# Kernel optimization log

Hardware: AMD Instinct MI355X
Metric: run time of the kernel (lower is better)

## Reference

```python
import jax, jax.numpy as jnp
import numpy as np
from jax import lax

# DCNv2 (ModulatedDeformConvPack) constants per init_kwargs
STRIDE, PAD, DIL, DG, KH, KW = 1, 1, 1, 1, 3, 3
K = KH * KW


def setup_inputs() -> dict:
    key = jax.random.key(0)
    k0, k1, k2 = jax.random.split(key, 3)
    B, C, H, W = 2, 64, 128, 128
    O = 64
    x = jax.random.normal(k0, (B, C, H, W), jnp.float32)
    weight = jax.random.normal(k1, (O, C, KH, KW), jnp.float32) / np.sqrt(C * KH * KW)
    bias = jnp.zeros((O,), jnp.float32)
    # small scale so predicted offsets stay within a few pixels (realistic trained DCN)
    offset_w = jax.random.normal(k2, (DG * 3 * K, C, KH, KW), jnp.float32) * 0.01
    offset_b = jnp.zeros((DG * 3 * K,), jnp.float32)
    return {"x": x, "weight": weight, "bias": bias, "offset_w": offset_w, "offset_b": offset_b}


def _modulated_deform_conv(x, weight, bias, offset_w, offset_b):
    B, C, H, W = x.shape
    O = weight.shape[0]
    # 1) offset/mask prediction conv (standard conv, same geometry as main conv)
    off = lax.conv_general_dilated(
        x, offset_w, window_strides=(STRIDE, STRIDE), padding=((PAD, PAD), (PAD, PAD)),
        rhs_dilation=(DIL, DIL), dimension_numbers=("NCHW", "OIHW", "NCHW"))
    off = off + offset_b[None, :, None, None]
    Ho, Wo = off.shape[2], off.shape[3]
    o1, o2, m = jnp.split(off, 3, axis=1)
    dy = o1.reshape(B, DG, K, Ho, Wo)
    dx = o2.reshape(B, DG, K, Ho, Wo)
    mask = jax.nn.sigmoid(m).reshape(B, DG, K, Ho, Wo)

    # 2) sampling positions: p = p0 + k*dil - pad + offset
    ki, kj = jnp.meshgrid(jnp.arange(KH), jnp.arange(KW), indexing="ij")
    base_y = (jnp.arange(Ho) * STRIDE - PAD)[None, :, None] + (ki.reshape(K) * DIL)[:, None, None]  # (K,Ho,1)
    base_x = (jnp.arange(Wo) * STRIDE - PAD)[None, None, :] + (kj.reshape(K) * DIL)[:, None, None]  # (K,1,Wo)
    py = base_y[None, None].astype(x.dtype) + dy  # (B,DG,K,Ho,Wo)
    px = base_x[None, None].astype(x.dtype) + dx

    y0 = jnp.floor(py)
    x0 = jnp.floor(px)
    wy = py - y0  # fractional weights
    wx = px - x0
    y0i = y0.astype(jnp.int32)
    x0i = x0.astype(jnp.int32)

    Cg = C // DG
    xg = x.reshape(B, DG, Cg, H * W)

    def corner(yi, xi):
        valid = ((yi >= 0) & (yi < H) & (xi >= 0) & (xi < W)).astype(x.dtype)  # zero-pad outside
        idx = jnp.clip(yi, 0, H - 1) * W + jnp.clip(xi, 0, W - 1)  # (B,DG,K,Ho,Wo)
        gather = lambda xf, id_: xf[:, id_]  # (Cg, K, Ho, Wo)
        vals = jax.vmap(jax.vmap(gather))(xg, idx)  # (B,DG,Cg,K,Ho,Wo)
        return vals * valid[:, :, None]

    wy_ = wy[:, :, None]
    wx_ = wx[:, :, None]
    samp = (corner(y0i, x0i) * (1 - wy_) * (1 - wx_)
            + corner(y0i, x0i + 1) * (1 - wy_) * wx_
            + corner(y0i + 1, x0i) * wy_ * (1 - wx_)
            + corner(y0i + 1, x0i + 1) * wy_ * wx_)
    samp = samp * mask[:, :, None]  # modulation
    samp = samp.reshape(B, C, K, Ho, Wo)

    # 3) contraction with conv weight (groups=1)
    out = jnp.einsum("bckhw,ock->bohw", samp, weight.reshape(O, C, K))
    return out + bias[None, :, None, None]


def reference(x, weight, bias, offset_w, offset_b):
    return _modulated_deform_conv(x, weight, bias, offset_w, offset_b)
```

## Files before the change

kernel.cpp:

```cpp
#include <hip/hip_runtime.h>
#include <hip/hip_bf16.h>

typedef __attribute__((ext_vector_type(8))) short bf16x8;
typedef __attribute__((ext_vector_type(4))) float f32x4;

#define Bc 2
#define Cc 64
#define Hc 128
#define Wc 128
#define Oc 64
#define NOFF 27
#define HWc (Hc * Wc)

__device__ __forceinline__ short f2bf(float f) {
    __hip_bfloat16 h = __float2bfloat16(f);
    return __builtin_bit_cast(short, h);
}
__device__ __forceinline__ float bf2f(short s) {
    __hip_bfloat16 h = __builtin_bit_cast(__hip_bfloat16, s);
    return __bfloat162float(h);
}

__global__ __launch_bounds__(256) void prep_kernel(
    const float* __restrict__ x, const float* __restrict__ w, const float* __restrict__ ow,
    short* __restrict__ xT, short* __restrict__ Ahi, short* __restrict__ Ohi) {
    int bid = blockIdx.x;
    int t = threadIdx.x;
    if (bid < 512) {
        int b = bid >> 8, rem = bid & 255;
        int h = rem >> 1, w0 = (rem & 1) << 6;
        __shared__ float tile[64][68];
        {
            int c = t >> 2, sub = t & 3;
            const float* src = x + ((size_t)(b * Cc + c) * Hc + h) * Wc + w0 + sub * 16;
#pragma unroll
            for (int j = 0; j < 4; ++j)
                *(float4*)&tile[c][sub * 16 + 4 * j] = *(const float4*)(src + 4 * j);
        }
        __syncthreads();
        {
            int ww = t >> 2, cs = (t & 3) << 4;
            short* dst = xT + (((size_t)(b * Hc + h)) * Wc + w0 + ww) * Cc + cs;
            bf16x8 v0, v1;
#pragma unroll
            for (int j = 0; j < 8; ++j) {
                v0[j] = f2bf(tile[cs + j][ww]);
                v1[j] = f2bf(tile[cs + 8 + j][ww]);
            }
            *(bf16x8*)(dst) = v0;
            *(bf16x8*)(dst + 8) = v1;
        }
    } else {
        int idx = (bid - 512) * 256 + t;
        const int NM = 4 * 18 * 64 * 8;
        const int NO = 2 * 18 * 64 * 8;
        if (idx < NM) {
            int j = idx & 7, lane = (idx >> 3) & 63, ks = (idx >> 9) % 18, mt = idx / 9216;
            int o  = mt * 16 + (lane & 15);
            int kk = ks >> 1;
            int c  = (ks & 1) * 32 + (lane >> 4) * 8 + j;
            Ahi[idx] = f2bf(w[(o * Cc + c) * 9 + kk]);
        } else if (idx < NM + NO) {
            int t2 = idx - NM;
            int j = t2 & 7, lane = (t2 >> 3) & 63, ks = (t2 >> 9) % 18, mt = t2 / 9216;
            int o  = mt * 16 + (lane & 15);
            int kk = ks >> 1;
            int c  = (ks & 1) * 32 + (lane >> 4) * 8 + j;
            Ohi[t2] = f2bf((o < NOFF) ? ow[(o * Cc + c) * 9 + kk] : 0.f);
        }
    }
}

__global__ __launch_bounds__(256, 2) void fused_dcn_kernel(
    const short* __restrict__ xT,
    const short* __restrict__ Ahi, const short* __restrict__ Ohi,
    const float* __restrict__ bias, const float* __restrict__ obias,
    float* __restrict__ out) {
    int bid = blockIdx.x;
    int b = bid >> 8, rem = bid & 255;
    int h = rem >> 1, w0 = (rem & 1) << 6;
    int tid = threadIdx.x;
    int lane = tid & 63, wv = tid >> 6;
    int n_loc = lane & 15, quad = lane >> 4;
    int p_glob = wv * 16 + n_loc;
    int wpix = w0 + p_glob;
    int cb0 = quad * 8, cb1 = 32 + quad * 8;

    __shared__ __align__(16) short Asm[2 * 18 * 64 * 8];
    __shared__ float4 wgt[576];
    __shared__ int4   sidx[576];
    __shared__ float  tmp[NOFF * 64];

    const short* xb = xT + (size_t)b * HWc * Cc;

    f32x4 oacc0 = {0.f, 0.f, 0.f, 0.f}, oacc1 = {0.f, 0.f, 0.f, 0.f};
    bf16x8 s1A[2], s1B[2];
    {
        int yc = min(max(h - 1, 0), Hc - 1);
        int xc = min(max(wpix - 1, 0), Wc - 1);
        const short* base = xb + ((size_t)yc * Wc + xc) * Cc;
        s1A[0] = *(const bf16x8*)(base + cb0);
        s1A[1] = *(const bf16x8*)(base + cb1);
    }
#pragma unroll
    for (int kk = 0; kk < 9; ++kk) {
        bf16x8* cur = (kk & 1) ? s1B : s1A;
        bf16x8* nxt = (kk & 1) ? s1A : s1B;
        if (kk < 8) {
            int kk2 = kk + 1;
            int yc = min(max(h + kk2 / 3 - 1, 0), Hc - 1);
            int xc = min(max(wpix + kk2 % 3 - 1, 0), Wc - 1);
            const short* base = xb + ((size_t)yc * Wc + xc) * Cc;
            nxt[0] = *(const bf16x8*)(base + cb0);
            nxt[1] = *(const bf16x8*)(base + cb1);
        }
        int y = h + kk / 3 - 1, xw = wpix + kk % 3 - 1;
        bool val = ((unsigned)y < (unsigned)Hc) && ((unsigned)xw < (unsigned)Wc);
        bf16x8 z = {0, 0, 0, 0, 0, 0, 0, 0};
        bf16x8 b0 = val ? cur[0] : z;
        bf16x8 b1 = val ? cur[1] : z;
#pragma unroll
        for (int ks = 0; ks < 2; ++ks) {
            bf16x8 bf = ks ? b1 : b0;
            int ksg = kk * 2 + ks;
            bf16x8 ah0 = *(const bf16x8*)(Ohi + ((0 * 18 + ksg) * 64 + lane) * 8);
            oacc0 = __builtin_amdgcn_mfma_f32_16x16x32_bf16(ah0, bf, oacc0, 0, 0, 0);
            bf16x8 ah1 = *(const bf16x8*)(Ohi + ((1 * 18 + ksg) * 64 + lane) * 8);
            oacc1 = __builtin_amdgcn_mfma_f32_16x16x32_bf16(ah1, bf, oacc1, 0, 0, 0);
        }
    }
    {
        int mrow = quad * 4;
#pragma unroll
        for (int r = 0; r < 4; ++r) {
            int oc = mrow + r;
            if (oc < NOFF) tmp[oc * 64 + p_glob] = oacc0[r] + obias[oc];
            int oc2 = 16 + mrow + r;
            if (oc2 < NOFF) tmp[oc2 * 64 + p_glob] = oacc1[r] + obias[oc2];
        }
    }
    for (int i = tid; i < 2304; i += 256)
        *((bf16x8*)Asm + i) = *((const bf16x8*)Ahi + i);
    __syncthreads();

    for (int t = tid; t < 576; t += 256) {
        int k = t >> 6, p = t & 63;
        float dy = tmp[k * 64 + p];
        float dx = tmp[(9 + k) * 64 + p];
        float mm = tmp[(18 + k) * 64 + p];
        float m  = 1.f / (1.f + __expf(-mm));
        float py = (float)(h - 1 + k / 3) + dy;
        float px = (float)(w0 + p - 1 + k % 3) + dx;
        float y0f = floorf(py), x0f = floorf(px);
        float fy = py - y0f, fx = px - x0f;
        int y0 = (int)y0f, x0i = (int)x0f;
        float vy0 = (y0 >= 0 && y0 < Hc) ? 1.f : 0.f;
        float vy1 = (y0 + 1 >= 0 && y0 + 1 < Hc) ? 1.f : 0.f;
        float vx0 = (x0i >= 0 && x0i < Wc) ? 1.f : 0.f;
        float vx1 = (x0i + 1 >= 0 && x0i + 1 < Wc) ? 1.f : 0.f;
        wgt[t] = make_float4((1.f - fy) * (1.f - fx) * m * vy0 * vx0,
                             (1.f - fy) * fx         * m * vy0 * vx1,
                             fy         * (1.f - fx) * m * vy1 * vx0,
                             fy         * fx         * m * vy1 * vx1);
        int cy0 = min(max(y0, 0), Hc - 1) * Wc;
        int cy1 = min(max(y0 + 1, 0), Hc - 1) * Wc;
        int cx0 = min(max(x0i, 0), Wc - 1);
        int cx1 = min(max(x0i + 1, 0), Wc - 1);
        sidx[t] = make_int4(cy0 + cx0, cy0 + cx1, cy1 + cx0, cy1 + cx1);
    }
    __syncthreads();

    f32x4 acc[4] = {{0.f, 0.f, 0.f, 0.f}, {0.f, 0.f, 0.f, 0.f},
                    {0.f, 0.f, 0.f, 0.f}, {0.f, 0.f, 0.f, 0.f}};
    bf16x8 bufA[8], bufB[8];
    float4 w4 = wgt[p_glob];
    {
        int4 id = sidx[p_glob];
        const short* c00 = xb + (size_t)id.x * Cc;
        const short* c01 = xb + (size_t)id.y * Cc;
        const short* c10 = xb + (size_t)id.z * Cc;
        const short* c11 = xb + (size_t)id.w * Cc;
        bufA[0] = *(const bf16x8*)(c00 + cb0); bufA[1] = *(const bf16x8*)(c00 + cb1);
        bufA[2] = *(const bf16x8*)(c01 + cb0); bufA[3] = *(const bf16x8*)(c01 + cb1);
        bufA[4] = *(const bf16x8*)(c10 + cb0); bufA[5] = *(const bf16x8*)(c10 + cb1);
        bufA[6] = *(const bf16x8*)(c11 + cb0); bufA[7] = *(const bf16x8*)(c11 + cb1);
    }
#pragma unroll
    for (int kk = 0; kk < 9; ++kk) {
        bf16x8* cur = (kk & 1) ? bufB : bufA;
        bf16x8* nxt = (kk & 1) ? bufA : bufB;
        float4 w4n = w4;
        if (kk < 8) {
            int4 idn = sidx[(kk + 1) * 64 + p_glob];
            w4n = wgt[(kk + 1) * 64 + p_glob];
            const short* c00 = xb + (size_t)idn.x * Cc;
            const short* c01 = xb + (size_t)idn.y * Cc;
            const short* c10 = xb + (size_t)idn.z * Cc;
            const short* c11 = xb + (size_t)idn.w * Cc;
            nxt[0] = *(const bf16x8*)(c00 + cb0); nxt[1] = *(const bf16x8*)(c00 + cb1);
            nxt[2] = *(const bf16x8*)(c01 + cb0); nxt[3] = *(const bf16x8*)(c01 + cb1);
            nxt[4] = *(const bf16x8*)(c10 + cb0); nxt[5] = *(const bf16x8*)(c10 + cb1);
            nxt[6] = *(const bf16x8*)(c11 + cb0); nxt[7] = *(const bf16x8*)(c11 + cb1);
        }
        bf16x8 b0, b1;
#pragma unroll
        for (int j = 0; j < 8; ++j) {
            float s0 = w4.x * bf2f(cur[0][j]) + w4.y * bf2f(cur[2][j])
                     + w4.z * bf2f(cur[4][j]) + w4.w * bf2f(cur[6][j]);
            float s1 = w4.x * bf2f(cur[1][j]) + w4.y * bf2f(cur[3][j])
                     + w4.z * bf2f(cur[5][j]) + w4.w * bf2f(cur[7][j]);
            b0[j] = f2bf(s0);
            b1[j] = f2bf(s1);
        }
#pragma unroll
        for (int ks = 0; ks < 2; ++ks) {
            bf16x8 bf = ks ? b1 : b0;
            int ksg = kk * 2 + ks;
            bf16x8 a0 = *(const bf16x8*)(Asm + ((0 * 18 + ksg) * 64 + lane) * 8);
            acc[0] = __builtin_amdgcn_mfma_f32_16x16x32_bf16(a0, bf, acc[0], 0, 0, 0);
            bf16x8 a1 = *(const bf16x8*)(Asm + ((1 * 18 + ksg) * 64 + lane) * 8);
            acc[1] = __builtin_amdgcn_mfma_f32_16x16x32_bf16(a1, bf, acc[1], 0, 0, 0);
            bf16x8 a2 = *(const bf16x8*)(Ahi + ((2 * 18 + ksg) * 64 + lane) * 8);
            acc[2] = __builtin_amdgcn_mfma_f32_16x16x32_bf16(a2, bf, acc[2], 0, 0, 0);
            bf16x8 a3 = *(const bf16x8*)(Ahi + ((3 * 18 + ksg) * 64 + lane) * 8);
            acc[3] = __builtin_amdgcn_mfma_f32_16x16x32_bf16(a3, bf, acc[3], 0, 0, 0);
        }
        w4 = w4n;
    }

    int mrow = quad * 4;
    float* ob = out + ((size_t)b * Oc * Hc + h) * Wc + w0 + p_glob;
#pragma unroll
    for (int mt = 0; mt < 4; ++mt)
#pragma unroll
        for (int r = 0; r < 4; ++r) {
            int o = mt * 16 + mrow + r;
            ob[(size_t)o * HWc] = acc[mt][r] + bias[o];
        }
}

extern "C" void kernel_launch(void* const* d_in, const int* in_sizes, int n_in,
                              void* d_out, int out_size, void* d_ws, size_t ws_size,
                              hipStream_t stream) {
    const float* x        = (const float*)d_in[0];
    const float* weight   = (const float*)d_in[1];
    const float* bias     = (const float*)d_in[2];
    const float* offset_w = (const float*)d_in[3];
    const float* offset_b = (const float*)d_in[4];
    float* out = (float*)d_out;

    char* ws = (char*)d_ws;
    short* xT  = (short*)(ws + 0);
    short* Ahi = (short*)(ws + 4194304);
    short* Ohi = (short*)(ws + 4268032);

    prep_kernel<<<512 + 216, 256, 0, stream>>>(x, weight, offset_w, xT, Ahi, Ohi);
    fused_dcn_kernel<<<Bc * Hc * 2, 256, 0, stream>>>(xT, Ahi, Ohi, bias, offset_b, out);
}
```

Measured before the change: 99.36 us.

## Split kernel taps across two wave groups with LDS reduction (split-K)

Doubles the block to 512 threads, with each half handling a subset of the 9 kernel taps (0-3 and 4-8) in both the offset conv and the deformable sampling and MFMA stage. Partial accumulators are reduced through shared memory before the offset post-processing and again before the output store. This is meant to raise wave-level parallelism and hide gather latency on a grid of only 512 blocks. In exchange it adds extra barriers, LDS traffic for the reductions, and uneven work between the two halves.

```diff
diff --git a/kernel.cpp b/kernel.cpp
--- a/kernel.cpp
+++ b/kernel.cpp
@@ -71,7 +71,111 @@
     }
 }
 
-__global__ __launch_bounds__(256, 2) void fused_dcn_kernel(
+template<int KB, int KE>
+__device__ __forceinline__ void stage1_taps(
+    const short* __restrict__ xb, const short* __restrict__ Ohi,
+    int h, int wpix, int lane, int cb0, int cb1, f32x4& oacc0, f32x4& oacc1) {
+    bf16x8 bA[2], bB[2];
+    {
+        int yc = min(max(h + KB / 3 - 1, 0), Hc - 1);
+        int xc = min(max(wpix + KB % 3 - 1, 0), Wc - 1);
+        const short* base = xb + ((size_t)yc * Wc + xc) * Cc;
+        bA[0] = *(const bf16x8*)(base + cb0);
+        bA[1] = *(const bf16x8*)(base + cb1);
+    }
+#pragma unroll
+    for (int kk = KB; kk < KE; ++kk) {
+        bf16x8* cur = ((kk - KB) & 1) ? bB : bA;
+        bf16x8* nxt = ((kk - KB) & 1) ? bA : bB;
+        if (kk < KE - 1) {
+            int kk2 = kk + 1;
+            int yc = min(max(h + kk2 / 3 - 1, 0), Hc - 1);
+            int xc = min(max(wpix + kk2 % 3 - 1, 0), Wc - 1);
+            const short* base = xb + ((size_t)yc * Wc + xc) * Cc;
+            nxt[0] = *(const bf16x8*)(base + cb0);
+            nxt[1] = *(const bf16x8*)(base + cb1);
+        }
+        int y = h + kk / 3 - 1, xw = wpix + kk % 3 - 1;
+        bool val = ((unsigned)y < (unsigned)Hc) && ((unsigned)xw < (unsigned)Wc);
+        bf16x8 z = {0, 0, 0, 0, 0, 0, 0, 0};
+        bf16x8 b0 = val ? cur[0] : z;
+        bf16x8 b1 = val ? cur[1] : z;
+#pragma unroll
+        for (int ks = 0; ks < 2; ++ks) {
+            bf16x8 bf = ks ? b1 : b0;
+            int ksg = kk * 2 + ks;
+            bf16x8 ah0 = *(const bf16x8*)(Ohi + ((0 * 18 + ksg) * 64 + lane) * 8);
+            oacc0 = __builtin_amdgcn_mfma_f32_16x16x32_bf16(ah0, bf, oacc0, 0, 0, 0);
+            bf16x8 ah1 = *(const bf16x8*)(Ohi + ((1 * 18 + ksg) * 64 + lane) * 8);
+            oacc1 = __builtin_amdgcn_mfma_f32_16x16x32_bf16(ah1, bf, oacc1, 0, 0, 0);
+        }
+    }
+}
+
+template<int KB, int KE>
+__device__ __forceinline__ void stage2_taps(
+    const short* __restrict__ xb, const short* __restrict__ Asm,
+    const short* __restrict__ Ahi, const float4* __restrict__ wgt,
+    const int4* __restrict__ sidx, int p_glob, int lane, int cb0, int cb1,
+    f32x4 acc[4]) {
+    bf16x8 bufA[8], bufB[8];
+    float4 w4 = wgt[KB * 64 + p_glob];
+    {
+        int4 id = sidx[KB * 64 + p_glob];
+        const short* c00 = xb + (size_t)id.x * Cc;
+        const short* c01 = xb + (size_t)id.y * Cc;
+        const short* c10 = xb + (size_t)id.z * Cc;
+        const short* c11 = xb + (size_t)id.w * Cc;
+        bufA[0] = *(const bf16x8*)(c00 + cb0); bufA[1] = *(const bf16x8*)(c00 + cb1);
+        bufA[2] = *(const bf16x8*)(c01 + cb0); bufA[3] = *(const bf16x8*)(c01 + cb1);
+        bufA[4] = *(const bf16x8*)(c10 + cb0); bufA[5] = *(const bf16x8*)(c10 + cb1);
+        bufA[6] = *(const bf16x8*)(c11 + cb0); bufA[7] = *(const bf16x8*)(c11 + cb1);
+    }
+#pragma unroll
+    for (int kk = KB; kk < KE; ++kk) {
+        bf16x8* cur = ((kk - KB) & 1) ? bufB : bufA;
+        bf16x8* nxt = ((kk - KB) & 1) ? bufA : bufB;
+        float4 w4n = w4;
+        if (kk < KE - 1) {
+            int4 idn = sidx[(kk + 1) * 64 + p_glob];
+            w4n = wgt[(kk + 1) * 64 + p_glob];
+            const short* c00 = xb + (size_t)idn.x * Cc;
+            const short* c01 = xb + (size_t)idn.y * Cc;
+            const short* c10 = xb + (size_t)idn.z * Cc;
+            const short* c11 = xb + (size_t)idn.w * Cc;
+            nxt[0] = *(const bf16x8*)(c00 + cb0); nxt[1] = *(const bf16x8*)(c00 + cb1);
+            nxt[2] = *(const bf16x8*)(c01 + cb0); nxt[3] = *(const bf16x8*)(c01 + cb1);
+            nxt[4] = *(const bf16x8*)(c10 + cb0); nxt[5] = *(const bf16x8*)(c10 + cb1);
+            nxt[6] = *(const bf16x8*)(c11 + cb0); nxt[7] = *(const bf16x8*)(c11 + cb1);
+        }
+        bf16x8 b0, b1;
+#pragma unroll
+        for (int j = 0; j < 8; ++j) {
+            float s0 = w4.x * bf2f(cur[0][j]) + w4.y * bf2f(cur[2][j])
+                     + w4.z * bf2f(cur[4][j]) + w4.w * bf2f(cur[6][j]);
+            float s1 = w4.x * bf2f(cur[1][j]) + w4.y * bf2f(cur[3][j])
+                     + w4.z * bf2f(cur[5][j]) + w4.w * bf2f(cur[7][j]);
+            b0[j] = f2bf(s0);
+            b1[j] = f2bf(s1);
+        }
+#pragma unroll
+        for (int ks = 0; ks < 2; ++ks) {
+            bf16x8 bf = ks ? b1 : b0;
+            int ksg = kk * 2 + ks;
+            bf16x8 a0 = *(const bf16x8*)(Asm + ((0 * 18 + ksg) * 64 + lane) * 8);
+            acc[0] = __builtin_amdgcn_mfma_f32_16x16x32_bf16(a0, bf, acc[0], 0, 0, 0);
+            bf16x8 a1 = *(const bf16x8*)(Asm + ((1 * 18 + ksg) * 64 + lane) * 8);
+            acc[1] = __builtin_amdgcn_mfma_f32_16x16x32_bf16(a1, bf, acc[1], 0, 0, 0);
+            bf16x8 a2 = *(const bf16x8*)(Ahi + ((2 * 18 + ksg) * 64 + lane) * 8);
+            acc[2] = __builtin_amdgcn_mfma_f32_16x16x32_bf16(a2, bf, acc[2], 0, 0, 0);
+            bf16x8 a3 = *(const bf16x8*)(Ahi + ((3 * 18 + ksg) * 64 + lane) * 8);
+            acc[3] = __builtin_amdgcn_mfma_f32_16x16x32_bf16(a3, bf, acc[3], 0, 0, 0);
+        }
+        w4 = w4n;
+    }
+}
+
+__global__ __launch_bounds__(512, 4) void fused_dcn_kernel(
     const short* __restrict__ xT,
     const short* __restrict__ Ahi, const short* __restrict__ Ohi,
     const float* __restrict__ bias, const float* __restrict__ obias,
@@ -80,70 +184,49 @@
     int b = bid >> 8, rem = bid & 255;
     int h = rem >> 1, w0 = (rem & 1) << 6;
     int tid = threadIdx.x;
-    int lane = tid & 63, wv = tid >> 6;
+    int lane = tid & 63, wav = tid >> 6;
+    int kg = wav >> 2, wv = wav & 3;
     int n_loc = lane & 15, quad = lane >> 4;
     int p_glob = wv * 16 + n_loc;
     int wpix = w0 + p_glob;
     int cb0 = quad * 8, cb1 = 32 + quad * 8;
 
-    __shared__ __align__(16) short Asm[2 * 18 * 64 * 8];
-    __shared__ float4 wgt[576];
-    __shared__ int4   sidx[576];
-    __shared__ float  tmp[NOFF * 64];
+    __shared__ __align__(16) char smem[62208];
+    short*  Asm  = (short*)smem;
+    float*  tmp  = (float*)(smem + 36864);
+    float4* wgt  = (float4*)(smem + 43776);
+    int4*   sidx = (int4*)(smem + 52992);
+    float*  red  = (float*)(smem + 43776);
 
     const short* xb = xT + (size_t)b * HWc * Cc;
 
     f32x4 oacc0 = {0.f, 0.f, 0.f, 0.f}, oacc1 = {0.f, 0.f, 0.f, 0.f};
-    bf16x8 s1A[2], s1B[2];
-    {
-        int yc = min(max(h - 1, 0), Hc - 1);
-        int xc = min(max(wpix - 1, 0), Wc - 1);
-        const short* base = xb + ((size_t)yc * Wc + xc) * Cc;
-        s1A[0] = *(const bf16x8*)(base + cb0);
-        s1A[1] = *(const bf16x8*)(base + cb1);
-    }
-#pragma unroll
-    for (int kk = 0; kk < 9; ++kk) {
-        bf16x8* cur = (kk & 1) ? s1B : s1A;
-        bf16x8* nxt = (kk & 1) ? s1A : s1B;
-        if (kk < 8) {
-            int kk2 = kk + 1;
-            int yc = min(max(h + kk2 / 3 - 1, 0), Hc - 1);
-            int xc = min(max(wpix + kk2 % 3 - 1, 0), Wc - 1);
-            const short* base = xb + ((size_t)yc * Wc + xc) * Cc;
-            nxt[0] = *(const bf16x8*)(base + cb0);
-            nxt[1] = *(const bf16x8*)(base + cb1);
-        }
-        int y = h + kk / 3 - 1, xw = wpix + kk % 3 - 1;
-        bool val = ((unsigned)y < (unsigned)Hc) && ((unsigned)xw < (unsigned)Wc);
-        bf16x8 z = {0, 0, 0, 0, 0, 0, 0, 0};
-        bf16x8 b0 = val ? cur[0] : z;
-        bf16x8 b1 = val ? cur[1] : z;
-#pragma unroll
-        for (int ks = 0; ks < 2; ++ks) {
-            bf16x8 bf = ks ? b1 : b0;
-            int ksg = kk * 2 + ks;
-            bf16x8 ah0 = *(const bf16x8*)(Ohi + ((0 * 18 + ksg) * 64 + lane) * 8);
-            oacc0 = __builtin_amdgcn_mfma_f32_16x16x32_bf16(ah0, bf, oacc0, 0, 0, 0);
-            bf16x8 ah1 = *(const bf16x8*)(Ohi + ((1 * 18 + ksg) * 64 + lane) * 8);
-            oacc1 = __builtin_amdgcn_mfma_f32_16x16x32_bf16(ah1, bf, oacc1, 0, 0, 0);
-        }
-    }
-    {
+    if (kg == 0) stage1_taps<0, 4>(xb, Ohi, h, wpix, lane, cb0, cb1, oacc0, oacc1);
+    else         stage1_taps<4, 9>(xb, Ohi, h, wpix, lane, cb0, cb1, oacc0, oacc1);
+
+    if (kg == 1) {
+        float* rp = red + (wv * 64 + lane) * 8;
+#pragma unroll
+        for (int r = 0; r < 4; ++r) { rp[r] = oacc0[r]; rp[4 + r] = oacc1[r]; }
+    }
+    for (int i = tid; i < 2304; i += 512)
+        *((bf16x8*)Asm + i) = *((const bf16x8*)Ahi + i);
+    __syncthreads();
+
+    if (kg == 0) {
+        const float* rp = red + (wv * 64 + lane) * 8;
         int mrow = quad * 4;
 #pragma unroll
         for (int r = 0; r < 4; ++r) {
             int oc = mrow + r;
-            if (oc < NOFF) tmp[oc * 64 + p_glob] = oacc0[r] + obias[oc];
+            if (oc < NOFF) tmp[oc * 64 + p_glob] = oacc0[r] + rp[r] + obias[oc];
             int oc2 = 16 + mrow + r;
-            if (oc2 < NOFF) tmp[oc2 * 64 + p_glob] = oacc1[r] + obias[oc2];
-        }
-    }
-    for (int i = tid; i < 2304; i += 256)
-        *((bf16x8*)Asm + i) = *((const bf16x8*)Ahi + i);
-    __syncthreads();
-
-    for (int t = tid; t < 576; t += 256) {
+            if (oc2 < NOFF) tmp[oc2 * 64 + p_glob] = oacc1[r] + rp[4 + r] + obias[oc2];
+        }
+    }
+    __syncthreads();
+
+    for (int t = tid; t < 576; t += 512) {
         int k = t >> 6, p = t & 63;
         float dy = tmp[k * 64 + p];
         float dx = tmp[(9 + k) * 64 + p];
@@ -172,71 +255,31 @@
 
     f32x4 acc[4] = {{0.f, 0.f, 0.f, 0.f}, {0.f, 0.f, 0.f, 0.f},
                     {0.f, 0.f, 0.f, 0.f}, {0.f, 0.f, 0.f, 0.f}};
-    bf16x8 bufA[8], bufB[8];
-    float4 w4 = wgt[p_glob];
-    {
-        int4 id = sidx[p_glob];
-        const short* c00 = xb + (size_t)id.x * Cc;
-        const short* c01 = xb + (size_t)id.y * Cc;
-        const short* c10 = xb + (size_t)id.z * Cc;
-        const short* c11 = xb + (size_t)id.w * Cc;
-        bufA[0] = *(const bf16x8*)(c00 + cb0); bufA[1] = *(const bf16x8*)(c00 + cb1);
-        bufA[2] = *(const bf16x8*)(c01 + cb0); bufA[3] = *(const bf16x8*)(c01 + cb1);
-        bufA[4] = *(const bf16x8*)(c10 + cb0); bufA[5] = *(const bf16x8*)(c10 + cb1);
-        bufA[6] = *(const bf16x8*)(c11 + cb0); bufA[7] = *(const bf16x8*)(c11 + cb1);
-    }
-#pragma unroll
-    for (int kk = 0; kk < 9; ++kk) {
-        bf16x8* cur = (kk & 1) ? bufB : bufA;
-        bf16x8* nxt = (kk & 1) ? bufA : bufB;
-        float4 w4n = w4;
-        if (kk < 8) {
-            int4 idn = sidx[(kk + 1) * 64 + p_glob];
-            w4n = wgt[(kk + 1) * 64 + p_glob];
-            const short* c00 = xb + (size_t)idn.x * Cc;
-            const short* c01 = xb + (size_t)idn.y * Cc;
-            const short* c10 = xb + (size_t)idn.z * Cc;
-            const short* c11 = xb + (size_t)idn.w * Cc;
-            nxt[0] = *(const bf16x8*)(c00 + cb0); nxt[1] = *(const bf16x8*)(c00 + cb1);
-            nxt[2] = *(const bf16x8*)(c01 + cb0); nxt[3] = *(const bf16x8*)(c01 + cb1);
-            nxt[4] = *(const bf16x8*)(c10 + cb0); nxt[5] = *(const bf16x8*)(c10 + cb1);
-            nxt[6] = *(const bf16x8*)(c11 + cb0); nxt[7] = *(const bf16x8*)(c11 + cb1);
-        }
-        bf16x8 b0, b1;
-#pragma unroll
-        for (int j = 0; j < 8; ++j) {
-            float s0 = w4.x * bf2f(cur[0][j]) + w4.y * bf2f(cur[2][j])
-                     + w4.z * bf2f(cur[4][j]) + w4.w * bf2f(cur[6][j]);
-            float s1 = w4.x * bf2f(cur[1][j]) + w4.y * bf2f(cur[3][j])
-                     + w4.z * bf2f(cur[5][j]) + w4.w * bf2f(cur[7][j]);
-            b0[j] = f2bf(s0);
-            b1[j] = f2bf(s1);
-        }
-#pragma unroll
-        for (int ks = 0; ks < 2; ++ks) {
-            bf16x8 bf = ks ? b1 : b0;
-            int ksg = kk * 2 + ks;
-            bf16x8 a0 = *(const bf16x8*)(Asm + ((0 * 18 + ksg) * 64 + lane) * 8);
-            acc[0] = __builtin_amdgcn_mfma_f32_16x16x32_bf16(a0, bf, acc[0], 0, 0, 0);
-            bf16x8 a1 = *(const bf16x8*)(Asm + ((1 * 18 + ksg) * 64 + lane) * 8);
-            acc[1] = __builtin_amdgcn_mfma_f32_16x16x32_bf16(a1, bf, acc[1], 0, 0, 0);
-            bf16x8 a2 = *(const bf16x8*)(Ahi + ((2 * 18 + ksg) * 64 + lane) * 8);
-            acc[2] = __builtin_amdgcn_mfma_f32_16x16x32_bf16(a2, bf, acc[2], 0, 0, 0);
-            bf16x8 a3 = *(const bf16x8*)(Ahi + ((3 * 18 + ksg) * 64 + lane) * 8);
-            acc[3] = __builtin_amdgcn_mfma_f32_16x16x32_bf16(a3, bf, acc[3], 0, 0, 0);
-        }
-        w4 = w4n;
-    }
-
-    int mrow = quad * 4;
-    float* ob = out + ((size_t)b * Oc * Hc + h) * Wc + w0 + p_glob;
-#pragma unroll
-    for (int mt = 0; mt < 4; ++mt)
-#pragma unroll
-        for (int r = 0; r < 4; ++r) {
-            int o = mt * 16 + mrow + r;
-            ob[(size_t)o * HWc] = acc[mt][r] + bias[o];
-        }
+    if (kg == 0) stage2_taps<0, 4>(xb, Asm, Ahi, wgt, sidx, p_glob, lane, cb0, cb1, acc);
+    else         stage2_taps<4, 9>(xb, Asm, Ahi, wgt, sidx, p_glob, lane, cb0, cb1, acc);
+
+    __syncthreads();
+    if (kg == 1) {
+        float* rp = red + (wv * 64 + lane) * 16;
+#pragma unroll
+        for (int mt = 0; mt < 4; ++mt)
+#pragma unroll
+            for (int r = 0; r < 4; ++r) rp[mt * 4 + r] = acc[mt][r];
+    }
+    __syncthreads();
+
+    if (kg == 0) {
+        const float* rp = red + (wv * 64 + lane) * 16;
+        int mrow = quad * 4;
+        float* ob = out + ((size_t)b * Oc * Hc + h) * Wc + w0 + p_glob;
+#pragma unroll
+        for (int mt = 0; mt < 4; ++mt)
+#pragma unroll
+            for (int r = 0; r < 4; ++r) {
+                int o = mt * 16 + mrow + r;
+                ob[(size_t)o * HWc] = acc[mt][r] + rp[mt * 4 + r] + bias[o];
+            }
+    }
 }
 
 extern "C" void kernel_launch(void* const* d_in, const int* in_sizes, int n_in,
@@ -255,5 +298,5 @@
     short* Ohi = (short*)(ws + 4268032);
 
     prep_kernel<<<512 + 216, 256, 0, stream>>>(x, weight, offset_w, xT, Ahi, Ohi);
-    fused_dcn_kernel<<<Bc * Hc * 2, 256, 0, stream>>>(xT, Ahi, Ohi, bias, offset_b, out);
-}
+    fused_dcn_kernel<<<Bc * Hc * 2, 512, 0, stream>>>(xT, Ahi, Ohi, bias, offset_b, out);
+}
```

After: 97.29 us. 2.1% less time.
